# Optimization experiments

Hardware: AMD Instinct MI355X
Metric: run time of the kernel (lower is better)

The kernel has to match this reference:

```python
import jax, jax.numpy as jnp
import numpy as np
from jax import lax

ALPHA = 0.1
N = 1024      # gallery size
J = 4         # number of embed blocks (2048 / 512)
BLOCK = 512

def setup_inputs() -> dict:
    key = jax.random.key(0)
    k1, k2, k3, k4 = jax.random.split(key, 4)
    x = jax.random.normal(k1, (N, 1024), dtype=jnp.float32)
    Wb = jax.random.normal(k2, (1024, 2048), dtype=jnp.float32) / np.sqrt(1024.0)
    W_embed = jax.random.normal(k3, (J, BLOCK, BLOCK, 2), dtype=jnp.float32) / BLOCK
    b_embed = jax.random.normal(k4, (J, 2), dtype=jnp.float32)
    return {"x": x, "Wb": Wb, "W_embed": W_embed, "b_embed": b_embed}

def _forward(x, Wb, W_embed, b_embed):
    alpha = ALPHA
    feats = x @ Wb                                   # [N, 2048]
    n = feats.shape[0]
    xb = feats.reshape(n, J, BLOCK).transpose(1, 0, 2)  # [J, N, BLOCK]
    # pairwise bilinear scores per block: S[j, a, b, k] = x_j[a] W_jk x_j[b] + b_jk
    S = jnp.einsum('jac,jcdk,jbd->jabk', xb, W_embed, xb) + b_embed[:, None, None, :]
    # transition matrices built from detached scores (g_g_score.data.clone())
    Sg = lax.stop_gradient(S)
    diag_mask = jnp.eye(n, dtype=bool)[None, :, :, None]     # [1, N, N, 1]
    masked = jnp.where(diag_mask, -jnp.inf, Sg)
    A = jax.nn.softmax(masked, axis=2)               # row softmax, [J, N, N, 2]
    A = jnp.transpose(A, (0, 3, 1, 2))               # [J, 2, N, N]
    I_N = jnp.eye(n, dtype=S.dtype)
    # closed-form personalized-PageRank diffusion, batched over (J, 2)
    A_an = (1.0 - alpha) * jnp.linalg.inv(I_N - alpha * A)  # [J, 2, N, N]
    # s[a,c] = sum_b p[a,b] * A[c,b]  (torch: p @ A.T)
    one = alpha * jnp.einsum('jabk,ikcb->jiack', S, A) + (1.0 - alpha) * S[:, None]
    ana = jnp.einsum('jabk,ikcb->jiack', S, A_an)
    out = jnp.concatenate([one.reshape(J, J, n * n, 2),
                           ana.reshape(J, J, n * n, 2)], axis=2)
    return out.reshape(-1, 2)

def reference(x, Wb, W_embed, b_embed):
    return _forward(x, Wb, W_embed, b_embed)
```

## Files before the change

### kernel.cpp

```cpp
#include <hip/hip_runtime.h>

#define NDIM 1024
#define MB (1ull<<20)

using f32x4  = __attribute__((ext_vector_type(4))) float;
using bf16x8 = __attribute__((ext_vector_type(8))) __bf16;
using u16x8  = __attribute__((ext_vector_type(8))) unsigned short;

__device__ __forceinline__ float bf2f(unsigned short u){
  union{unsigned int i; float f;} x; x.i = ((unsigned int)u)<<16; return x.f;
}
__device__ __forceinline__ unsigned short f2bf(float f){
  union{float fl; unsigned int i;} u; u.fl = f;
  unsigned int x = u.i;
  return (unsigned short)((x + 0x7fffu + ((x>>16)&1u)) >> 16);
}

__device__ __forceinline__ void gload16(const unsigned short* g, unsigned short* l){
  __builtin_amdgcn_global_load_lds(
      (const __attribute__((address_space(1))) void*)g,
      (__attribute__((address_space(3))) void*)l,
      16, 0, 0);
}


__global__ void k_split_x(const float* __restrict__ x, unsigned short* __restrict__ hi,
                          unsigned short* __restrict__ lo){
  size_t idx = ((size_t)blockIdx.x*256 + threadIdx.x)*4;
  float4 v = *(const float4*)(x+idx);
  float vv[4] = {v.x, v.y, v.z, v.w};
  ushort4 h, l;
  unsigned short* hp = (unsigned short*)&h;
  unsigned short* lp = (unsigned short*)&l;
  #pragma unroll
  for (int s=0;s<4;s++){
    unsigned short hb = f2bf(vv[s]);
    hp[s] = hb;
    lp[s] = f2bf(vv[s] - bf2f(hb));
  }
  *(ushort4*)(hi+idx) = h;
  *(ushort4*)(lo+idx) = l;
}

__global__ void k_trans_split(const float* __restrict__ Wb, unsigned short* __restrict__ hi,
                              unsigned short* __restrict__ lo){
  __shared__ float t[32][33];
  int bd = blockIdx.x, bc = blockIdx.y;
  int tx = threadIdx.x, ty = threadIdx.y;
  #pragma unroll
  for (int r=0;r<4;r++){
    int c = bc*32 + ty + r*8;
    t[ty+r*8][tx] = Wb[(size_t)c*2048 + bd*32 + tx];
  }
  __syncthreads();
  #pragma unroll
  for (int r=0;r<4;r++){
    int d = bd*32 + ty + r*8, c = bc*32 + tx;
    float v = t[tx][ty+r*8];
    unsigned short h = f2bf(v);
    hi[(size_t)d*1024 + c] = h;
    lo[(size_t)d*1024 + c] = f2bf(v - bf2f(h));
  }
}

__global__ void k_wt(const float* __restrict__ W, unsigned short* __restrict__ WT){
  __shared__ float t[32][33];
  int z = blockIdx.z; int j = z>>1, k = z&1;
  int bd = blockIdx.x, bc = blockIdx.y;
  int tx = threadIdx.x, ty = threadIdx.y;
  #pragma unroll
  for (int r=0;r<4;r++){
    int c = bc*32 + ty + r*8, d = bd*32 + tx;
    t[ty+r*8][tx] = W[(((size_t)j*512 + c)*512 + d)*2 + k];
  }
  __syncthreads();
  #pragma unroll
  for (int r=0;r<4;r++){
    int d = bd*32 + ty + r*8, c = bc*32 + tx;
    WT[((size_t)z*512 + d)*512 + c] = f2bf(t[tx][ty+r*8]);
  }
}

__global__ void k_softmax(const unsigned short* __restrict__ S, unsigned short* __restrict__ A){
  int z = blockIdx.y, c = blockIdx.x, t = threadIdx.x;
  const unsigned short* row = S + ((size_t)z*NDIM + c)*NDIM;
  __shared__ float red[256];
  float v[4];
  float mx = -1e30f;
  #pragma unroll
  for (int s=0;s<4;s++){
    int b = t + s*256;
    float x = bf2f(row[b]);
    if (b==c) x = -1e30f;
    v[s] = x; mx = fmaxf(mx, x);
  }
  red[t]=mx; __syncthreads();
  for (int o=128;o>0;o>>=1){ if (t<o) red[t]=fmaxf(red[t],red[t+o]); __syncthreads(); }
  mx = red[0]; __syncthreads();
  float e[4]; float sum=0.f;
  #pragma unroll
  for (int s=0;s<4;s++){ e[s] = __expf(v[s]-mx); sum += e[s]; }
  red[t]=sum; __syncthreads();
  for (int o=128;o>0;o>>=1){ if (t<o) red[t]+=red[t+o]; __syncthreads(); }
  sum = red[0];
  float inv = 1.0f/sum;
  unsigned short* Ar = A + ((size_t)z*NDIM + c)*NDIM;
  #pragma unroll
  for (int s=0;s<4;s++){
    int b = t + s*256;
    Ar[b] = f2bf(e[s]*inv);
  }
}

__global__ void k_transb(const unsigned short* __restrict__ A, unsigned short* __restrict__ AT){
  __shared__ unsigned short t[64][65];
  int z = blockIdx.z, bb = blockIdx.x, bc = blockIdx.y;
  int tx = threadIdx.x, ty = threadIdx.y;
  const unsigned short* Az = A + (size_t)z*NDIM*NDIM;
  #pragma unroll
  for (int r=0;r<16;r++){
    int c = bc*64 + ty + r*4;
    t[ty+r*4][tx] = Az[(size_t)c*NDIM + bb*64 + tx];
  }
  __syncthreads();
  unsigned short* Tz = AT + (size_t)z*NDIM*NDIM;
  #pragma unroll
  for (int r=0;r<16;r++){
    int b = bb*64 + ty + r*4;
    Tz[(size_t)b*NDIM + bc*64 + tx] = t[tx][ty+r*4];
  }
}

__global__ void k_combine(const unsigned short* __restrict__ A, const unsigned short* __restrict__ A2,
                          const unsigned short* __restrict__ A3, unsigned short* __restrict__ Aan){
  size_t idx = ((size_t)blockIdx.x*256 + threadIdx.x)*8;
  int cb = (int)(idx & ((size_t)NDIM*NDIM - 1));
  int c = cb >> 10, b0 = cb & 1023;
  u16x8 a  = *(const u16x8*)(A+idx);
  u16x8 a2 = *(const u16x8*)(A2+idx);
  u16x8 a3 = *(const u16x8*)(A3+idx);
  u16x8 o;
  #pragma unroll
  for (int s=0;s<8;s++){
    float v = 0.1f*bf2f(a[s]) + 0.01f*bf2f(a2[s]) + 0.001f*bf2f(a3[s]);
    if (b0+s == c) v += 1.0f;
    o[s] = f2bf(0.9f*v);
  }
  *(u16x8*)(Aan+idx) = o;
}


struct GemmP {
  const unsigned short* Aseg[3]; const unsigned short* Bseg[3];
  long long sA, sB;
  int zShiftA, zShiftB;
  int lda, ldb;
  int K, tilesN;
  unsigned short* Cb; long long sCb; int ldcb;
  const unsigned short* Sroot;
  const float* bias;
  float* outp;
  float scale, scale2;
};

template<int EPI, int NSEG>
__global__ __launch_bounds__(256) void k_gemm(GemmP p){
  const int z = blockIdx.y;
  const int tm = blockIdx.x / p.tilesN;
  const int tn = blockIdx.x % p.tilesN;
  int jj=0, ii=0, kk=0;
  size_t zoffA, zoffB;
  if (EPI==4 || EPI==5){
    jj = z>>3; ii = (z>>1)&3; kk = z&1;
    zoffA = (size_t)(jj*2+kk)*(size_t)p.sA;
    zoffB = (size_t)(ii*2+kk)*(size_t)p.sB;
  } else {
    zoffA = (size_t)(z>>p.zShiftA)*(size_t)p.sA;
    zoffB = (size_t)(z>>p.zShiftB)*(size_t)p.sB;
  }
  __shared__ unsigned short As[128*32];
  __shared__ unsigned short Bs[128*32];
  const int t = threadIdx.x;
  const int lane = t & 63;
  const int w = t >> 6;
  const int wm = w >> 1, wn = w & 1;

  f32x4 acc[4][4];
  #pragma unroll
  for (int m=0;m<4;m++)
    #pragma unroll
    for (int n=0;n<4;n++)
      acc[m][n] = (f32x4)(0.0f);

  const int srow = w*32 + (lane>>2);
  const int swz  = ((lane&3) ^ ((srow>>1)&3)) * 8;
  const size_t aoff0 = (size_t)(tm*128 + srow)*p.lda + swz;
  const size_t aoff1 = (size_t)(tm*128 + srow + 16)*p.lda + swz;
  const size_t boff0 = (size_t)(tn*128 + srow)*p.ldb + swz;
  const size_t boff1 = (size_t)(tn*128 + srow + 16)*p.ldb + swz;
  unsigned short* lA0 = &As[w*1024];
  unsigned short* lA1 = &As[w*1024 + 512];
  unsigned short* lB0 = &Bs[w*1024];
  unsigned short* lB1 = &Bs[w*1024 + 512];

  const int rb = lane & 15, g = lane >> 4;
  const int rswz = (g ^ ((rb>>1)&3)) * 8;

  #pragma unroll
  for (int s=0;s<NSEG;s++){
    const unsigned short* ga = p.Aseg[s] + zoffA;
    const unsigned short* gb = p.Bseg[s] + zoffB;
    for (int k0=0; k0<p.K; k0+=32){
      __syncthreads();
      gload16(ga + aoff0 + k0, lA0);
      gload16(ga + aoff1 + k0, lA1);
      gload16(gb + boff0 + k0, lB0);
      gload16(gb + boff1 + k0, lB1);
      __syncthreads();
      bf16x8 af[4], bfr[4];
      #pragma unroll
      for (int m=0;m<4;m++) af[m]  = *(const bf16x8*)&As[(wm*64 + m*16 + rb)*32 + rswz];
      #pragma unroll
      for (int n=0;n<4;n++) bfr[n] = *(const bf16x8*)&Bs[(wn*64 + n*16 + rb)*32 + rswz];
      #pragma unroll
      for (int m=0;m<4;m++)
        #pragma unroll
        for (int n=0;n<4;n++)
          acc[m][n] = __builtin_amdgcn_mfma_f32_16x16x32_bf16(af[m], bfr[n], acc[m][n], 0, 0, 0);
    }
  }

  const int rl = (lane>>4)*4;
  const int cl = lane & 15;
  const int row0 = tm*128 + wm*64;
  const int col0 = tn*128 + wn*64;
  #pragma unroll
  for (int m=0;m<4;m++){
    #pragma unroll
    for (int n=0;n<4;n++){
      #pragma unroll
      for (int r=0;r<4;r++){
        const int row = row0 + m*16 + rl + r;
        const int col = col0 + n*16 + cl;
        float v = acc[m][n][r];
        if (EPI==2){
          float nv = p.scale*v + (p.bias ? p.bias[z] : 0.0f);
          p.Cb[(size_t)z*p.sCb + (size_t)row*p.ldcb + col] = f2bf(nv);
        } else if (EPI==4){
          float add = p.scale2 * bf2f(p.Sroot[(size_t)(jj*2+kk)*(size_t)p.sA + (size_t)row*p.lda + col]);
          size_t ob = (size_t)(jj*4+ii)*(2ull*NDIM*NDIM)*2 + (size_t)kk;
          p.outp[ob + ((size_t)row*NDIM + col)*2] = p.scale*v + add;
        } else if (EPI==5){
          size_t ob = (size_t)(jj*4+ii)*(2ull*NDIM*NDIM)*2 + (size_t)kk;
          p.outp[ob + ((size_t)((size_t)NDIM*NDIM + (size_t)row*NDIM + col))*2] = p.scale*v;
        }
      }
    }
  }
}


extern "C" void kernel_launch(void* const* d_in, const int* in_sizes, int n_in,
                              void* d_out, int out_size, void* d_ws, size_t ws_size,
                              hipStream_t stream){
  (void)in_sizes; (void)n_in; (void)out_size; (void)ws_size;
  const float* x  = (const float*)d_in[0];
  const float* Wb = (const float*)d_in[1];
  const float* We = (const float*)d_in[2];
  const float* be = (const float*)d_in[3];
  float* out = (float*)d_out;
  char* ws = (char*)d_ws;

  unsigned short* xhi   = (unsigned short*)(ws + 0);
  unsigned short* xlo   = (unsigned short*)(ws + 2*MB);
  unsigned short* wbth  = (unsigned short*)(ws + 4*MB);
  unsigned short* wbtl  = (unsigned short*)(ws + 8*MB);
  unsigned short* featb = (unsigned short*)(ws + 12*MB);
  unsigned short* WT    = (unsigned short*)(ws + 16*MB);
  unsigned short* Tb    = (unsigned short*)(ws + 20*MB);
  unsigned short* Sb    = (unsigned short*)(ws + 28*MB);
  unsigned short* Abuf  = (unsigned short*)(ws + 44*MB);
  unsigned short* ATb   = (unsigned short*)(ws + 60*MB);
  unsigned short* A2b   = (unsigned short*)(ws + 76*MB);
  unsigned short* A3b   = (unsigned short*)(ws + 92*MB);
  unsigned short* Aan   = (unsigned short*)(ws + 108*MB);

  k_split_x<<<dim3(1024), dim3(256), 0, stream>>>(x, xhi, xlo);
  k_trans_split<<<dim3(64,32), dim3(32,8), 0, stream>>>(Wb, wbth, wbtl);
  k_wt<<<dim3(16,16,8), dim3(32,8), 0, stream>>>(We, WT);

  {
    GemmP q{};
    q.Aseg[0]=xhi; q.Bseg[0]=wbth;
    q.Aseg[1]=xhi; q.Bseg[1]=wbtl;
    q.Aseg[2]=xlo; q.Bseg[2]=wbth;
    q.sA = 0; q.sB = 0; q.zShiftA = 0; q.zShiftB = 0;
    q.lda = 1024; q.ldb = 1024; q.K = 1024; q.tilesN = 16;
    q.Cb = featb; q.sCb = 0; q.ldcb = 2048;
    q.bias = nullptr; q.scale = 1.0f;
    k_gemm<2,3><<<dim3(8*16,1), dim3(256), 0, stream>>>(q);
  }

  {
    GemmP q{};
    q.Aseg[0] = featb; q.sA = 512; q.zShiftA = 1; q.lda = 2048;
    q.Bseg[0] = WT;    q.sB = (long long)512*512; q.zShiftB = 0; q.ldb = 512;
    q.K = 512; q.tilesN = 4;
    q.Cb = Tb; q.sCb = (long long)1024*512; q.ldcb = 512;
    q.bias = nullptr; q.scale = 1.0f;
    k_gemm<2,1><<<dim3(8*4,8), dim3(256), 0, stream>>>(q);
  }

  {
    GemmP q{};
    q.Aseg[0] = Tb;    q.sA = (long long)1024*512; q.zShiftA = 0; q.lda = 512;
    q.Bseg[0] = featb; q.sB = 512; q.zShiftB = 1; q.ldb = 2048;
    q.K = 512; q.tilesN = 8;
    q.Cb = Sb; q.sCb = (long long)NDIM*NDIM; q.ldcb = 1024;
    q.bias = be; q.scale = 1.0f;
    k_gemm<2,1><<<dim3(8*8,8), dim3(256), 0, stream>>>(q);
  }

  k_softmax<<<dim3(1024,8), dim3(256), 0, stream>>>(Sb, Abuf);
  k_transb<<<dim3(16,16,8), dim3(64,4), 0, stream>>>(Abuf, ATb);

  auto pgemm = [&](const unsigned short* Aop, unsigned short* dst){
    GemmP q{};
    q.Aseg[0] = Aop; q.sA = (long long)NDIM*NDIM; q.zShiftA = 0; q.lda = 1024;
    q.Bseg[0] = ATb; q.sB = (long long)NDIM*NDIM; q.zShiftB = 0; q.ldb = 1024;
    q.K = 1024; q.tilesN = 8;
    q.Cb = dst; q.sCb = (long long)NDIM*NDIM; q.ldcb = 1024;
    q.bias = nullptr; q.scale = 1.0f;
    k_gemm<2,1><<<dim3(8*8,8), dim3(256), 0, stream>>>(q);
  };
  pgemm(Abuf, A2b);
  pgemm(A2b,  A3b);

  k_combine<<<dim3(4096), dim3(256), 0, stream>>>(Abuf, A2b, A3b, Aan);

  {
    GemmP q{};
    q.Aseg[0] = Sb;   q.sA = (long long)NDIM*NDIM; q.lda = 1024;
    q.Bseg[0] = Abuf; q.sB = (long long)NDIM*NDIM; q.ldb = 1024;
    q.K = 1024; q.tilesN = 8;
    q.Sroot = Sb; q.outp = out;
    q.scale = 0.1f; q.scale2 = 0.9f;
    k_gemm<4,1><<<dim3(8*8,32), dim3(256), 0, stream>>>(q);
  }
  {
    GemmP q{};
    q.Aseg[0] = Sb;  q.sA = (long long)NDIM*NDIM; q.lda = 1024;
    q.Bseg[0] = Aan; q.sB = (long long)NDIM*NDIM; q.ldb = 1024;
    q.K = 1024; q.tilesN = 8;
    q.outp = out;
    q.scale = 1.0f; q.scale2 = 0.0f;
    k_gemm<5,1><<<dim3(8*8,32), dim3(256), 0, stream>>>(q);
  }
}
```

Measured before the change: 697.3 us.

## Double-buffer GEMM LDS tiles and fuse both k-channels in output GEMMs

The generic GEMM now uses two LDS buffers so the next K-slice's global-to-LDS load is issued before the MFMA work on the current slice, leaving one barrier per step instead of two. The two output GEMMs get a dedicated kernel that computes the k=0 and k=1 channels in one block with two accumulator sets. Each output element is then written as one float2 store instead of two strided scalar stores. This doubles LDS use and raises register pressure, which can lower occupancy. The launch_bounds(256,2) hint on the fused kernel may cause register spills.

```diff
diff --git a/kernel.cpp b/kernel.cpp
--- a/kernel.cpp
+++ b/kernel.cpp
@@ -1,6 +1,7 @@
 #include <hip/hip_runtime.h>
 
 #define NDIM 1024
+#define NN (1024ull*1024ull)
 #define MB (1ull<<20)
 
 using f32x4  = __attribute__((ext_vector_type(4))) float;
@@ -116,14 +117,14 @@
   __shared__ unsigned short t[64][65];
   int z = blockIdx.z, bb = blockIdx.x, bc = blockIdx.y;
   int tx = threadIdx.x, ty = threadIdx.y;
-  const unsigned short* Az = A + (size_t)z*NDIM*NDIM;
+  const unsigned short* Az = A + (size_t)z*NN;
   #pragma unroll
   for (int r=0;r<16;r++){
     int c = bc*64 + ty + r*4;
     t[ty+r*4][tx] = Az[(size_t)c*NDIM + bb*64 + tx];
   }
   __syncthreads();
-  unsigned short* Tz = AT + (size_t)z*NDIM*NDIM;
+  unsigned short* Tz = AT + (size_t)z*NN;
   #pragma unroll
   for (int r=0;r<16;r++){
     int b = bb*64 + ty + r*4;
@@ -134,7 +135,7 @@
 __global__ void k_combine(const unsigned short* __restrict__ A, const unsigned short* __restrict__ A2,
                           const unsigned short* __restrict__ A3, unsigned short* __restrict__ Aan){
   size_t idx = ((size_t)blockIdx.x*256 + threadIdx.x)*8;
-  int cb = (int)(idx & ((size_t)NDIM*NDIM - 1));
+  int cb = (int)(idx & (NN - 1));
   int c = cb >> 10, b0 = cb & 1023;
   u16x8 a  = *(const u16x8*)(A+idx);
   u16x8 a2 = *(const u16x8*)(A2+idx);
@@ -157,29 +158,19 @@
   int lda, ldb;
   int K, tilesN;
   unsigned short* Cb; long long sCb; int ldcb;
-  const unsigned short* Sroot;
   const float* bias;
-  float* outp;
-  float scale, scale2;
+  float scale;
 };
 
-template<int EPI, int NSEG>
+template<int NSEG>
 __global__ __launch_bounds__(256) void k_gemm(GemmP p){
   const int z = blockIdx.y;
   const int tm = blockIdx.x / p.tilesN;
   const int tn = blockIdx.x % p.tilesN;
-  int jj=0, ii=0, kk=0;
-  size_t zoffA, zoffB;
-  if (EPI==4 || EPI==5){
-    jj = z>>3; ii = (z>>1)&3; kk = z&1;
-    zoffA = (size_t)(jj*2+kk)*(size_t)p.sA;
-    zoffB = (size_t)(ii*2+kk)*(size_t)p.sB;
-  } else {
-    zoffA = (size_t)(z>>p.zShiftA)*(size_t)p.sA;
-    zoffB = (size_t)(z>>p.zShiftB)*(size_t)p.sB;
-  }
-  __shared__ unsigned short As[128*32];
-  __shared__ unsigned short Bs[128*32];
+  const size_t zoffA = (size_t)(z>>p.zShiftA)*(size_t)p.sA;
+  const size_t zoffB = (size_t)(z>>p.zShiftB)*(size_t)p.sB;
+  __shared__ unsigned short As[2][4096];
+  __shared__ unsigned short Bs[2][4096];
   const int t = threadIdx.x;
   const int lane = t & 63;
   const int w = t >> 6;
@@ -198,65 +189,168 @@
   const size_t aoff1 = (size_t)(tm*128 + srow + 16)*p.lda + swz;
   const size_t boff0 = (size_t)(tn*128 + srow)*p.ldb + swz;
   const size_t boff1 = (size_t)(tn*128 + srow + 16)*p.ldb + swz;
-  unsigned short* lA0 = &As[w*1024];
-  unsigned short* lA1 = &As[w*1024 + 512];
-  unsigned short* lB0 = &Bs[w*1024];
-  unsigned short* lB1 = &Bs[w*1024 + 512];
+
+  const int kpseg = p.K >> 5;
+  const int nt = kpseg * NSEG;
+
+  auto stage = [&](int step, int buf){
+    const int seg = (NSEG==1) ? 0 : (step / kpseg);
+    const int k0 = (step - seg*kpseg) << 5;
+    const unsigned short* ga = p.Aseg[seg] + zoffA;
+    const unsigned short* gb = p.Bseg[seg] + zoffB;
+    gload16(ga + aoff0 + k0, &As[buf][w*1024]);
+    gload16(ga + aoff1 + k0, &As[buf][w*1024+512]);
+    gload16(gb + boff0 + k0, &Bs[buf][w*1024]);
+    gload16(gb + boff1 + k0, &Bs[buf][w*1024+512]);
+  };
 
   const int rb = lane & 15, g = lane >> 4;
   const int rswz = (g ^ ((rb>>1)&3)) * 8;
 
-  #pragma unroll
-  for (int s=0;s<NSEG;s++){
-    const unsigned short* ga = p.Aseg[s] + zoffA;
-    const unsigned short* gb = p.Bseg[s] + zoffB;
-    for (int k0=0; k0<p.K; k0+=32){
-      __syncthreads();
-      gload16(ga + aoff0 + k0, lA0);
-      gload16(ga + aoff1 + k0, lA1);
-      gload16(gb + boff0 + k0, lB0);
-      gload16(gb + boff1 + k0, lB1);
-      __syncthreads();
-      bf16x8 af[4], bfr[4];
-      #pragma unroll
-      for (int m=0;m<4;m++) af[m]  = *(const bf16x8*)&As[(wm*64 + m*16 + rb)*32 + rswz];
-      #pragma unroll
-      for (int n=0;n<4;n++) bfr[n] = *(const bf16x8*)&Bs[(wn*64 + n*16 + rb)*32 + rswz];
-      #pragma unroll
-      for (int m=0;m<4;m++)
-        #pragma unroll
-        for (int n=0;n<4;n++)
-          acc[m][n] = __builtin_amdgcn_mfma_f32_16x16x32_bf16(af[m], bfr[n], acc[m][n], 0, 0, 0);
-    }
+  stage(0, 0);
+  __syncthreads();
+  int cur = 0;
+  for (int s=0; s<nt; ++s){
+    if (s+1 < nt) stage(s+1, cur^1);
+    bf16x8 af[4], bfr[4];
+    #pragma unroll
+    for (int m=0;m<4;m++) af[m]  = *(const bf16x8*)&As[cur][(wm*64 + m*16 + rb)*32 + rswz];
+    #pragma unroll
+    for (int n=0;n<4;n++) bfr[n] = *(const bf16x8*)&Bs[cur][(wn*64 + n*16 + rb)*32 + rswz];
+    #pragma unroll
+    for (int m=0;m<4;m++)
+      #pragma unroll
+      for (int n=0;n<4;n++)
+        acc[m][n] = __builtin_amdgcn_mfma_f32_16x16x32_bf16(af[m], bfr[n], acc[m][n], 0, 0, 0);
+    __syncthreads();
+    cur ^= 1;
   }
 
   const int rl = (lane>>4)*4;
   const int cl = lane & 15;
   const int row0 = tm*128 + wm*64;
   const int col0 = tn*128 + wn*64;
-  #pragma unroll
-  for (int m=0;m<4;m++){
-    #pragma unroll
-    for (int n=0;n<4;n++){
+  const float bz = p.bias ? p.bias[z] : 0.0f;
+  #pragma unroll
+  for (int m=0;m<4;m++)
+    #pragma unroll
+    for (int n=0;n<4;n++)
       #pragma unroll
       for (int r=0;r<4;r++){
         const int row = row0 + m*16 + rl + r;
         const int col = col0 + n*16 + cl;
-        float v = acc[m][n][r];
-        if (EPI==2){
-          float nv = p.scale*v + (p.bias ? p.bias[z] : 0.0f);
-          p.Cb[(size_t)z*p.sCb + (size_t)row*p.ldcb + col] = f2bf(nv);
-        } else if (EPI==4){
-          float add = p.scale2 * bf2f(p.Sroot[(size_t)(jj*2+kk)*(size_t)p.sA + (size_t)row*p.lda + col]);
-          size_t ob = (size_t)(jj*4+ii)*(2ull*NDIM*NDIM)*2 + (size_t)kk;
-          p.outp[ob + ((size_t)row*NDIM + col)*2] = p.scale*v + add;
-        } else if (EPI==5){
-          size_t ob = (size_t)(jj*4+ii)*(2ull*NDIM*NDIM)*2 + (size_t)kk;
-          p.outp[ob + ((size_t)((size_t)NDIM*NDIM + (size_t)row*NDIM + col))*2] = p.scale*v;
+        p.Cb[(size_t)z*p.sCb + (size_t)row*p.ldcb + col] = f2bf(p.scale*acc[m][n][r] + bz);
+      }
+}
+
+struct OutP {
+  const unsigned short* Sp;
+  const unsigned short* Bp;
+  float* outp;
+};
+
+template<bool WITH_S>
+__global__ __launch_bounds__(256,2) void k_out(OutP p){
+  const int zi = blockIdx.y;
+  const int jj = zi >> 2, ii = zi & 3;
+  const int tm = blockIdx.x >> 3, tn = blockIdx.x & 7;
+  const unsigned short* A0 = p.Sp + (size_t)(jj*2+0)*NN;
+  const unsigned short* A1 = p.Sp + (size_t)(jj*2+1)*NN;
+  const unsigned short* B0 = p.Bp + (size_t)(ii*2+0)*NN;
+  const unsigned short* B1 = p.Bp + (size_t)(ii*2+1)*NN;
+  __shared__ unsigned short As[2][2][4096];
+  __shared__ unsigned short Bs[2][2][4096];
+  const int t = threadIdx.x;
+  const int lane = t & 63;
+  const int w = t >> 6;
+  const int wm = w >> 1, wn = w & 1;
+
+  f32x4 acc0[4][4], acc1[4][4];
+  #pragma unroll
+  for (int m=0;m<4;m++)
+    #pragma unroll
+    for (int n=0;n<4;n++){
+      acc0[m][n] = (f32x4)(0.0f);
+      acc1[m][n] = (f32x4)(0.0f);
+    }
+
+  const int srow = w*32 + (lane>>2);
+  const int swz  = ((lane&3) ^ ((srow>>1)&3)) * 8;
+  const size_t aoff0 = (size_t)(tm*128 + srow)*1024 + swz;
+  const size_t aoff1 = (size_t)(tm*128 + srow + 16)*1024 + swz;
+  const size_t boff0 = (size_t)(tn*128 + srow)*1024 + swz;
+  const size_t boff1 = (size_t)(tn*128 + srow + 16)*1024 + swz;
+
+  auto stage = [&](int step, int buf){
+    const int k0 = step << 5;
+    gload16(A0 + aoff0 + k0, &As[buf][0][w*1024]);
+    gload16(A0 + aoff1 + k0, &As[buf][0][w*1024+512]);
+    gload16(A1 + aoff0 + k0, &As[buf][1][w*1024]);
+    gload16(A1 + aoff1 + k0, &As[buf][1][w*1024+512]);
+    gload16(B0 + boff0 + k0, &Bs[buf][0][w*1024]);
+    gload16(B0 + boff1 + k0, &Bs[buf][0][w*1024+512]);
+    gload16(B1 + boff0 + k0, &Bs[buf][1][w*1024]);
+    gload16(B1 + boff1 + k0, &Bs[buf][1][w*1024+512]);
+  };
+
+  const int rb = lane & 15, g = lane >> 4;
+  const int rswz = (g ^ ((rb>>1)&3)) * 8;
+
+  stage(0, 0);
+  __syncthreads();
+  int cur = 0;
+  for (int s=0; s<32; ++s){
+    if (s+1 < 32) stage(s+1, cur^1);
+    {
+      bf16x8 af[4], bfr[4];
+      #pragma unroll
+      for (int m=0;m<4;m++) af[m]  = *(const bf16x8*)&As[cur][0][(wm*64 + m*16 + rb)*32 + rswz];
+      #pragma unroll
+      for (int n=0;n<4;n++) bfr[n] = *(const bf16x8*)&Bs[cur][0][(wn*64 + n*16 + rb)*32 + rswz];
+      #pragma unroll
+      for (int m=0;m<4;m++)
+        #pragma unroll
+        for (int n=0;n<4;n++)
+          acc0[m][n] = __builtin_amdgcn_mfma_f32_16x16x32_bf16(af[m], bfr[n], acc0[m][n], 0, 0, 0);
+    }
+    {
+      bf16x8 af[4], bfr[4];
+      #pragma unroll
+      for (int m=0;m<4;m++) af[m]  = *(const bf16x8*)&As[cur][1][(wm*64 + m*16 + rb)*32 + rswz];
+      #pragma unroll
+      for (int n=0;n<4;n++) bfr[n] = *(const bf16x8*)&Bs[cur][1][(wn*64 + n*16 + rb)*32 + rswz];
+      #pragma unroll
+      for (int m=0;m<4;m++)
+        #pragma unroll
+        for (int n=0;n<4;n++)
+          acc1[m][n] = __builtin_amdgcn_mfma_f32_16x16x32_bf16(af[m], bfr[n], acc1[m][n], 0, 0, 0);
+    }
+    __syncthreads();
+    cur ^= 1;
+  }
+
+  const int rl = (lane>>4)*4;
+  const int cl = lane & 15;
+  const int row0 = tm*128 + wm*64;
+  const int col0 = tn*128 + wn*64;
+  const size_t ob = (size_t)(jj*4+ii)*(4ull*NN) + (WITH_S ? 0 : 2ull*NN);
+  #pragma unroll
+  for (int m=0;m<4;m++)
+    #pragma unroll
+    for (int n=0;n<4;n++)
+      #pragma unroll
+      for (int r=0;r<4;r++){
+        const int row = row0 + m*16 + rl + r;
+        const int col = col0 + n*16 + cl;
+        float v0 = acc0[m][n][r];
+        float v1 = acc1[m][n][r];
+        if (WITH_S){
+          v0 = 0.1f*v0 + 0.9f*bf2f(A0[(size_t)row*1024 + col]);
+          v1 = 0.1f*v1 + 0.9f*bf2f(A1[(size_t)row*1024 + col]);
         }
+        float2 val; val.x = v0; val.y = v1;
+        *(float2*)(p.outp + ob + ((size_t)row*1024 + col)*2) = val;
       }
-    }
-  }
 }
 
 
@@ -298,7 +392,7 @@
     q.lda = 1024; q.ldb = 1024; q.K = 1024; q.tilesN = 16;
     q.Cb = featb; q.sCb = 0; q.ldcb = 2048;
     q.bias = nullptr; q.scale = 1.0f;
-    k_gemm<2,3><<<dim3(8*16,1), dim3(256), 0, stream>>>(q);
+    k_gemm<3><<<dim3(8*16,1), dim3(256), 0, stream>>>(q);
   }
 
   {
@@ -308,7 +402,7 @@
     q.K = 512; q.tilesN = 4;
     q.Cb = Tb; q.sCb = (long long)1024*512; q.ldcb = 512;
     q.bias = nullptr; q.scale = 1.0f;
-    k_gemm<2,1><<<dim3(8*4,8), dim3(256), 0, stream>>>(q);
+    k_gemm<1><<<dim3(8*4,8), dim3(256), 0, stream>>>(q);
   }
 
   {
@@ -316,9 +410,9 @@
     q.Aseg[0] = Tb;    q.sA = (long long)1024*512; q.zShiftA = 0; q.lda = 512;
     q.Bseg[0] = featb; q.sB = 512; q.zShiftB = 1; q.ldb = 2048;
     q.K = 512; q.tilesN = 8;
-    q.Cb = Sb; q.sCb = (long long)NDIM*NDIM; q.ldcb = 1024;
+    q.Cb = Sb; q.sCb = (long long)NN; q.ldcb = 1024;
     q.bias = be; q.scale = 1.0f;
-    k_gemm<2,1><<<dim3(8*8,8), dim3(256), 0, stream>>>(q);
+    k_gemm<1><<<dim3(8*8,8), dim3(256), 0, stream>>>(q);
   }
 
   k_softmax<<<dim3(1024,8), dim3(256), 0, stream>>>(Sb, Abuf);
@@ -326,12 +420,12 @@
 
   auto pgemm = [&](const unsigned short* Aop, unsigned short* dst){
     GemmP q{};
-    q.Aseg[0] = Aop; q.sA = (long long)NDIM*NDIM; q.zShiftA = 0; q.lda = 1024;
-    q.Bseg[0] = ATb; q.sB = (long long)NDIM*NDIM; q.zShiftB = 0; q.ldb = 1024;
+    q.Aseg[0] = Aop; q.sA = (long long)NN; q.zShiftA = 0; q.lda = 1024;
+    q.Bseg[0] = ATb; q.sB = (long long)NN; q.zShiftB = 0; q.ldb = 1024;
     q.K = 1024; q.tilesN = 8;
-    q.Cb = dst; q.sCb = (long long)NDIM*NDIM; q.ldcb = 1024;
+    q.Cb = dst; q.sCb = (long long)NN; q.ldcb = 1024;
     q.bias = nullptr; q.scale = 1.0f;
-    k_gemm<2,1><<<dim3(8*8,8), dim3(256), 0, stream>>>(q);
+    k_gemm<1><<<dim3(8*8,8), dim3(256), 0, stream>>>(q);
   };
   pgemm(Abuf, A2b);
   pgemm(A2b,  A3b);
@@ -339,21 +433,11 @@
   k_combine<<<dim3(4096), dim3(256), 0, stream>>>(Abuf, A2b, A3b, Aan);
 
   {
-    GemmP q{};
-    q.Aseg[0] = Sb;   q.sA = (long long)NDIM*NDIM; q.lda = 1024;
-    q.Bseg[0] = Abuf; q.sB = (long long)NDIM*NDIM; q.ldb = 1024;
-    q.K = 1024; q.tilesN = 8;
-    q.Sroot = Sb; q.outp = out;
-    q.scale = 0.1f; q.scale2 = 0.9f;
-    k_gemm<4,1><<<dim3(8*8,32), dim3(256), 0, stream>>>(q);
+    OutP q{Sb, Abuf, out};
+    k_out<true><<<dim3(64,16), dim3(256), 0, stream>>>(q);
   }
   {
-    GemmP q{};
-    q.Aseg[0] = Sb;  q.sA = (long long)NDIM*NDIM; q.lda = 1024;
-    q.Bseg[0] = Aan; q.sB = (long long)NDIM*NDIM; q.ldb = 1024;
-    q.K = 1024; q.tilesN = 8;
-    q.outp = out;
-    q.scale = 1.0f; q.scale2 = 0.0f;
-    k_gemm<5,1><<<dim3(8*8,32), dim3(256), 0, stream>>>(q);
-  }
-}
+    OutP q{Sb, Aan, out};
+    k_out<false><<<dim3(64,16), dim3(256), 0, stream>>>(q);
+  }
+}
```

New measurement: 659.3 us. 1.06x faster.
